# Kernel tuning notes

Measured on AMD Instinct MI355X. Metric: run time of the kernel, lower is better.

## Reference

```python
import jax, jax.numpy as jnp
import numpy as np

B, V = 4, 10242
N = B * V            # 40968 packed vertices
E_PER = 30720        # edges per mesh
HID = 128


def _bilinear_sample(fm, grid):
    """pytorch3d vert_align core: grid_sample(align_corners=True, bilinear).
    fm: [B,C,H,W], grid: [B,V,2] xy in [-1,1] -> [B,V,C]."""
    b_, c_, h_, w_ = fm.shape
    x = (grid[..., 0] + 1.0) * 0.5 * (w_ - 1)
    y = (grid[..., 1] + 1.0) * 0.5 * (h_ - 1)
    x0f, y0f = jnp.floor(x), jnp.floor(y)
    wx1, wy1 = x - x0f, y - y0f
    wx0, wy0 = 1.0 - wx1, 1.0 - wy1
    x0 = jnp.clip(x0f, 0, w_ - 1).astype(jnp.int32)
    x1 = jnp.clip(x0f + 1, 0, w_ - 1).astype(jnp.int32)
    y0 = jnp.clip(y0f, 0, h_ - 1).astype(jnp.int32)
    y1 = jnp.clip(y0f + 1, 0, h_ - 1).astype(jnp.int32)
    fmt = jnp.transpose(fm, (0, 2, 3, 1))  # [B,H,W,C]
    bi = jnp.arange(b_)[:, None]
    g = lambda yy, xx: fmt[bi, yy, xx]     # [B,V,C]
    return ((wy0 * wx0)[..., None] * g(y0, x0)
            + (wy0 * wx1)[..., None] * g(y0, x1)
            + (wy1 * wx0)[..., None] * g(y1, x0)
            + (wy1 * wx1)[..., None] * g(y1, x1))


def _graph_conv(x, edges, w0, b0, w1, b1):
    """pytorch3d GraphConv (undirected): W0 x_i + sum over both edge dirs of W1 x_j."""
    h0 = x @ w0 + b0
    h1 = x @ w1 + b1
    e0, e1 = edges[:, 0], edges[:, 1]
    agg = jnp.zeros_like(h0).at[e0].add(h1[e1]).at[e1].add(h1[e0])
    return h0 + agg


def setup_inputs() -> dict:
    key = jax.random.key(0)
    ks = jax.random.split(key, 20)
    s = 0.05
    # per-mesh edges, offset into packed index space
    e = jax.random.randint(ks[0], (B, E_PER, 2), 0, V)
    e = e + (jnp.arange(B) * V)[:, None, None]
    return {
        "feat1": jax.random.normal(ks[1], (B, 256, 56, 56), jnp.float32),
        "feat2": jax.random.normal(ks[2], (B, 512, 28, 28), jnp.float32),
        "feat3": jax.random.normal(ks[3], (B, 1024, 14, 14), jnp.float32),
        "feat4": jax.random.normal(ks[4], (B, 2048, 7, 7), jnp.float32),
        "aligned_verts": jax.random.uniform(ks[5], (B, V, 3), jnp.float32, -1.0, 1.0),
        "verts_packed": jax.random.normal(ks[6], (N, 3), jnp.float32),
        "image_enc": jax.random.normal(ks[7], (B, 256), jnp.float32),
        "edges": e.reshape(B * E_PER, 2).astype(jnp.int64),
        "bottleneck_w": jax.random.normal(ks[8], (3840, HID), jnp.float32) * s,
        "bottleneck_b": jnp.zeros((HID,), jnp.float32),
        "g0_w0": jax.random.normal(ks[9], (387, HID), jnp.float32) * s,
        "g0_b0": jnp.zeros((HID,), jnp.float32),
        "g0_w1": jax.random.normal(ks[10], (387, HID), jnp.float32) * s,
        "g0_b1": jnp.zeros((HID,), jnp.float32),
        "gw0": jax.random.normal(ks[11], (7, HID, HID), jnp.float32) * s,
        "gb0": jnp.zeros((7, HID), jnp.float32),
        "gw1": jax.random.normal(ks[12], (7, HID, HID), jnp.float32) * s,
        "gb1": jnp.zeros((7, HID), jnp.float32),
        "off_w": jax.random.normal(ks[13], (HID, 3), jnp.float32) * s,
        "off_b": jnp.zeros((3,), jnp.float32),
    }


def reference(feat1, feat2, feat3, feat4, aligned_verts, verts_packed, image_enc,
              edges, bottleneck_w, bottleneck_b, g0_w0, g0_b0, g0_w1, g0_b1,
              gw0, gb0, gw1, gb1, off_w, off_b):
    grid = aligned_verts[..., :2]  # vert_align uses xy only
    samp = jnp.concatenate([_bilinear_sample(f, grid)
                            for f in (feat1, feat2, feat3, feat4)], axis=-1)
    samp = samp.reshape(N, 3840)  # return_packed=True
    vfeat = jax.nn.relu(samp @ bottleneck_w + bottleneck_b)
    enc = jnp.repeat(image_enc, V, axis=0)  # repeat_interleave
    x = jnp.concatenate([vfeat, verts_packed, enc], axis=1)  # [N,387]
    x = jax.nn.relu(_graph_conv(x, edges, g0_w0, g0_b0, g0_w1, g0_b1))
    for i in range(7):
        x = jax.nn.relu(_graph_conv(x, edges, gw0[i], gb0[i], gw1[i], gb1[i]))
    return x @ off_w + off_b  # delta_v [N,3]
```

## Files before the change

### kernel.cpp

```cpp
#include <hip/hip_runtime.h>

static inline int ceil_div(int a, int b) { return (a + b - 1) / b; }

typedef __attribute__((ext_vector_type(8))) short short8;
typedef __attribute__((ext_vector_type(4))) float floatx4;

__device__ __forceinline__ unsigned short f2bf(float f) {
    unsigned int u = __float_as_uint(f);
    unsigned int r = (u + 0x7fffu + ((u >> 16) & 1u)) >> 16;
    return (unsigned short)r;
}
__device__ __forceinline__ float bf2f(unsigned short h) {
    return __uint_as_float(((unsigned int)h) << 16);
}

__global__ __launch_bounds__(1024) void scan1_k(const int* __restrict__ deg,
                                                int* __restrict__ excl,
                                                int* __restrict__ bsum, int Nv) {
    __shared__ int s[1024];
    int tid = threadIdx.x;
    int i = blockIdx.x * 1024 + tid;
    int v = (i < Nv) ? deg[i] : 0;
    s[tid] = v;
    __syncthreads();
    for (int off = 1; off < 1024; off <<= 1) {
        int t = (tid >= off) ? s[tid - off] : 0;
        __syncthreads();
        if (tid >= off) s[tid] += t;
        __syncthreads();
    }
    if (i < Nv) excl[i] = s[tid] - v;
    if (tid == 1023) bsum[blockIdx.x] = s[1023];
}

__global__ __launch_bounds__(64) void scan2_k(int* __restrict__ bsum, int nb) {
    __shared__ int s[64];
    int tid = threadIdx.x;
    int v = (tid < nb) ? bsum[tid] : 0;
    s[tid] = v;
    __syncthreads();
    for (int off = 1; off < 64; off <<= 1) {
        int t = (tid >= off) ? s[tid - off] : 0;
        __syncthreads();
        if (tid >= off) s[tid] += t;
        __syncthreads();
    }
    if (tid < nb) bsum[tid] = s[tid] - v;
}

__global__ __launch_bounds__(1024) void scan3_k(const int* __restrict__ excl,
                                                const int* __restrict__ bsum,
                                                const int* __restrict__ deg,
                                                int* __restrict__ rowptr,
                                                int* __restrict__ cursor, int Nv) {
    int i = blockIdx.x * 1024 + threadIdx.x;
    if (i < Nv) {
        int val = excl[i] + bsum[blockIdx.x];
        rowptr[i] = val;
        cursor[i] = val;
        if (i == Nv - 1) rowptr[Nv] = val + deg[i];
    }
}

__global__ __launch_bounds__(256) void fill_adj_k(const int* __restrict__ edges,
                                                  int* __restrict__ cursor,
                                                  int* __restrict__ adj, int E) {
    int e = blockIdx.x * blockDim.x + threadIdx.x;
    if (e < E) {
        int a = edges[2 * e], b = edges[2 * e + 1];
        adj[atomicAdd(&cursor[a], 1)] = b;
        adj[atomicAdd(&cursor[b], 1)] = a;
    }
}

__global__ __launch_bounds__(256) void fatpre_k(const int* __restrict__ edges,
                                                int* __restrict__ deg, int E, int nE,
                                                const float* __restrict__ g0w0,
                                                const float* __restrict__ g0w1,
                                                const float* __restrict__ gw0,
                                                const float* __restrict__ gw1,
                                                unsigned short* __restrict__ Wt,
                                                const float* __restrict__ bw,
                                                unsigned short* __restrict__ bwT,
                                                const float* __restrict__ enc,
                                                float* __restrict__ encp, int B_) {
    int bid = blockIdx.x;
    int tid = threadIdx.x;
    if (bid < nE) {
        int e = bid * 256 + tid;
        if (e < E) {
            atomicAdd(&deg[edges[2 * e]], 1);
            atomicAdd(&deg[edges[2 * e + 1]], 1);
        }
    } else if (bid < nE + 16) {
        int lh = bid - nE;
        int l = lh >> 1, h = lh & 1;
        const float* src;
        if (l == 0) src = h ? g0w1 : g0w0;
        else src = (h ? gw1 : gw0) + (size_t)(l - 1) * 16384;
        unsigned short* dst = Wt + (size_t)lh * 16384;
        for (int idx = tid; idx < 16384; idx += 256) {
            int n = idx >> 7, k = idx & 127;
            dst[n * 128 + k] = f2bf(src[k * 128 + n]);
        }
    } else if (bid < nE + 46) {
        int blk = bid - nE - 16;
        for (int idx = tid; idx < 16384; idx += 256) {
            int n = idx >> 7, kk = idx & 127;
            bwT[(size_t)n * 3840 + blk * 128 + kk] =
                f2bf(bw[(size_t)(blk * 128 + kk) * 128 + n]);
        }
    } else {
        int b = bid - nE - 46;
        int sH = tid >> 7;
        int j = tid & 127;
        const float* w = sH ? g0w1 : g0w0;
        const float* eb = enc + b * 256;
        float acc = 0.f;
        for (int c = 0; c < 256; ++c) acc = fmaf(eb[c], w[(131 + c) * 128 + j], acc);
        encp[(sH * B_ + b) * 128 + j] = acc;
    }
}

__global__ __launch_bounds__(256) void proj_all_k(
    const float* __restrict__ fm1, const float* __restrict__ fm2,
    const float* __restrict__ fm3, const float* __restrict__ fm4,
    const unsigned short* __restrict__ bwT, float* __restrict__ q1, float* __restrict__ q2,
    float* __restrict__ q3, float* __restrict__ q4, int B_) {
    __shared__ unsigned short wlds[8192];

    int tid = threadIdx.x;
    int n1 = 49 * B_ * 4, n2 = 13 * B_ * 8, n3 = 4 * B_ * 16;
    int bid = blockIdx.x;
    const float* fm;
    float* op;
    int C, HW, PT, idx, koff;
    if (bid < n1) {
        fm = fm1; op = q1; C = 256; HW = 3136; PT = 49; idx = bid; koff = 0;
    } else if (bid < n1 + n2) {
        fm = fm2; op = q2; C = 512; HW = 784; PT = 13; idx = bid - n1; koff = 256;
    } else if (bid < n1 + n2 + n3) {
        fm = fm3; op = q3; C = 1024; HW = 196; PT = 4; idx = bid - n1 - n2; koff = 768;
    } else {
        fm = fm4; op = q4; C = 2048; HW = 49; PT = 1; idx = bid - n1 - n2 - n3; koff = 1792;
    }
    int pt = idx % PT;
    int r2 = idx / PT;
    int b = r2 % B_;
    int zz = r2 / B_;
    int p0 = pt * 64;
    int S = B_ * HW * 128;
    const float* fmb = fm + (size_t)b * C * HW;
    int kcf = zz * 64;
    int kcw = koff + kcf;

#pragma unroll
    for (int l = 0; l < 4; ++l) {
        int i2 = tid + l * 256;
        int n = i2 >> 3, c16 = i2 & 7;
        *(short8*)&wlds[n * 64 + ((c16 ^ (n & 7)) * 8)] =
            *(const short8*)(bwT + (size_t)n * 3840 + kcw + c16 * 8);
    }

    int wave = tid >> 6, lane = tid & 63;
    int row16 = lane & 15, quad = lane >> 4;
    int p = p0 + wave * 16 + row16;
    bool pok = (p < HW);
    int pc = pok ? p : 0;
    short8 ax[2];
#pragma unroll
    for (int ks = 0; ks < 2; ++ks) {
#pragma unroll
        for (int j = 0; j < 8; ++j) {
            float v = pok ? fmb[(size_t)(kcf + ks * 32 + quad * 8 + j) * HW + pc] : 0.f;
            ax[ks][j] = (short)f2bf(v);
        }
    }
    __syncthreads();

    floatx4 acc[8];
#pragma unroll
    for (int j = 0; j < 8; ++j) acc[j] = (floatx4){0.f, 0.f, 0.f, 0.f};
#pragma unroll
    for (int ks = 0; ks < 2; ++ks) {
        int c = ks * 4 + quad;
#pragma unroll
        for (int nt = 0; nt < 8; ++nt) {
            int wr = nt * 16 + row16;
            short8 bwf = *(short8*)&wlds[wr * 64 + ((c ^ (wr & 7)) * 8)];
            acc[nt] = __builtin_amdgcn_mfma_f32_16x16x32_bf16(ax[ks], bwf, acc[nt], 0, 0, 0);
        }
    }

    float* obase = op + (size_t)zz * S + (size_t)b * HW * 128;
#pragma unroll
    for (int nt = 0; nt < 8; ++nt) {
        int colg = nt * 16 + row16;
#pragma unroll
        for (int rr = 0; rr < 4; ++rr) {
            int pr = p0 + wave * 16 + quad * 4 + rr;
            if (pr < HW) obase[(size_t)pr * 128 + colg] = acc[nt][rr];
        }
    }
}

__global__ __launch_bounds__(256) void reduce4_k(const float* __restrict__ q1,
                                                 const float* __restrict__ q2,
                                                 const float* __restrict__ q3,
                                                 const float* __restrict__ q4,
                                                 float* __restrict__ o1, float* __restrict__ o2,
                                                 float* __restrict__ o3, float* __restrict__ o4,
                                                 int S1, int S2, int S3, int S4) {
    int i = (blockIdx.x * 256 + threadIdx.x) * 4;
    const float* src;
    float* dst;
    int S, z, base;
    if (i < S1) {
        src = q1; dst = o1; S = S1; z = 4; base = i;
    } else if (i < S1 + S2) {
        src = q2; dst = o2; S = S2; z = 8; base = i - S1;
    } else if (i < S1 + S2 + S3) {
        src = q3; dst = o3; S = S3; z = 16; base = i - S1 - S2;
    } else if (i < S1 + S2 + S3 + S4) {
        src = q4; dst = o4; S = S4; z = 32; base = i - S1 - S2 - S3;
    } else {
        return;
    }
    float4 a = *(const float4*)(src + base);
    for (int zz = 1; zz < z; ++zz) {
        float4 b = *(const float4*)(src + (size_t)zz * S + base);
        a.x += b.x; a.y += b.y; a.z += b.z; a.w += b.w;
    }
    *(float4*)(dst + base) = a;
}

__device__ __forceinline__ float sample_level(const float* __restrict__ pp, int Hh, int Ww,
                                              float gx, float gy, int j) {
    float x = (gx + 1.f) * 0.5f * (float)(Ww - 1);
    float y = (gy + 1.f) * 0.5f * (float)(Hh - 1);
    float x0f = floorf(x), y0f = floorf(y);
    float wx1 = x - x0f, wy1 = y - y0f;
    float wx0 = 1.f - wx1, wy0 = 1.f - wy1;
    int x0 = (int)fminf(fmaxf(x0f, 0.f), (float)(Ww - 1));
    int x1 = (int)fminf(fmaxf(x0f + 1.f, 0.f), (float)(Ww - 1));
    int y0 = (int)fminf(fmaxf(y0f, 0.f), (float)(Hh - 1));
    int y1 = (int)fminf(fmaxf(y0f + 1.f, 0.f), (float)(Hh - 1));
    const float* r00 = pp + (size_t)(y0 * Ww + x0) * 128;
    const float* r01 = pp + (size_t)(y0 * Ww + x1) * 128;
    const float* r10 = pp + (size_t)(y1 * Ww + x0) * 128;
    const float* r11 = pp + (size_t)(y1 * Ww + x1) * 128;
    return wy0 * (wx0 * r00[j] + wx1 * r01[j]) + wy1 * (wx0 * r10[j] + wx1 * r11[j]);
}

__global__ __launch_bounds__(128) void sample_bottleneck_k(
    const float* __restrict__ av, const float* __restrict__ pp1, const float* __restrict__ pp2,
    const float* __restrict__ pp3, const float* __restrict__ pp4, const float* __restrict__ bb,
    const float* __restrict__ verts, const float* __restrict__ encp,
    const float* __restrict__ g0w0, const float* __restrict__ g0w1,
    const float* __restrict__ g0b0, const float* __restrict__ g0b1,
    unsigned short* __restrict__ X, unsigned short* __restrict__ H, int V_, int B_) {
    int n = blockIdx.x, j = threadIdx.x;
    int b = n / V_;
    float gx = av[(size_t)n * 3 + 0];
    float gy = av[(size_t)n * 3 + 1];
    float acc = bb[j];
    acc += sample_level(pp1 + (size_t)b * 3136 * 128, 56, 56, gx, gy, j);
    acc += sample_level(pp2 + (size_t)b * 784 * 128, 28, 28, gx, gy, j);
    acc += sample_level(pp3 + (size_t)b * 196 * 128, 14, 14, gx, gy, j);
    acc += sample_level(pp4 + (size_t)b * 49 * 128, 7, 7, gx, gy, j);
    X[(size_t)n * 128 + j] = f2bf(fmaxf(acc, 0.f));
    float v0 = verts[n * 3 + 0], v1 = verts[n * 3 + 1], v2 = verts[n * 3 + 2];
    float h0 = encp[(0 * B_ + b) * 128 + j] + g0b0[j] + v0 * g0w0[128 * 128 + j] +
               v1 * g0w0[129 * 128 + j] + v2 * g0w0[130 * 128 + j];
    float h1 = encp[(1 * B_ + b) * 128 + j] + g0b1[j] + v0 * g0w1[128 * 128 + j] +
               v1 * g0w1[129 * 128 + j] + v2 * g0w1[130 * 128 + j];
    H[(size_t)n * 256 + j] = f2bf(h0);
    H[(size_t)n * 256 + 128 + j] = f2bf(h1);
}

__device__ __forceinline__ int xcd_vertex(int bid, int wave, int V_, int B_, int Nv) {
    if (B_ == 4) {
        int xcd = bid & 7;
        int lb = (bid >> 3) * 2 + (xcd & 1);
        int lv = lb * 4 + wave;
        if (lv >= V_) return -1;
        return (xcd >> 1) * V_ + lv;
    }
    int n = bid * 4 + wave;
    return (n < Nv) ? n : -1;
}

__global__ __launch_bounds__(256) void aggpre_k(const unsigned short* __restrict__ H,
                                                const int* __restrict__ rowptr,
                                                const int* __restrict__ adj,
                                                float* __restrict__ pre, int Nv, int V_,
                                                int B_) {
    int wave = threadIdx.x >> 6, lane = threadIdx.x & 63;
    int n = xcd_vertex(blockIdx.x, wave, V_, B_, Nv);
    if (n < 0) return;
    unsigned int u = *(const unsigned int*)(H + (size_t)n * 256 + 2 * lane);
    float a0 = bf2f((unsigned short)(u & 0xffff));
    float a1 = bf2f((unsigned short)(u >> 16));
    int s = rowptr[n], e = rowptr[n + 1];
    for (int t = s; t < e; t += 8) {
        int nb[8];
        unsigned int w[8];
#pragma unroll
        for (int q = 0; q < 8; ++q) {
            int idx = (t + q < e) ? (t + q) : (e - 1);
            nb[q] = adj[idx];
        }
#pragma unroll
        for (int q = 0; q < 8; ++q)
            w[q] = *(const unsigned int*)(H + (size_t)nb[q] * 256 + 128 + 2 * lane);
#pragma unroll
        for (int q = 0; q < 8; ++q) {
            if (t + q < e) {
                a0 += bf2f((unsigned short)(w[q] & 0xffff));
                a1 += bf2f((unsigned short)(w[q] >> 16));
            }
        }
    }
    pre[(size_t)n * 128 + 2 * lane] = a0;
    pre[(size_t)n * 128 + 2 * lane + 1] = a1;
}

__global__ __launch_bounds__(256) void agg_x_k(const unsigned short* __restrict__ X,
                                               const int* __restrict__ rowptr,
                                               const int* __restrict__ adj,
                                               unsigned short* __restrict__ Agg, int Nv,
                                               int V_, int B_) {
    int wave = threadIdx.x >> 6, lane = threadIdx.x & 63;
    int n = xcd_vertex(blockIdx.x, wave, V_, B_, Nv);
    if (n < 0) return;
    const unsigned int* Xu = (const unsigned int*)X;
    float a0 = 0.f, a1 = 0.f;
    int s = rowptr[n], e = rowptr[n + 1];
    for (int t = s; t < e; t += 8) {
        int nb[8];
        unsigned int w[8];
#pragma unroll
        for (int q = 0; q < 8; ++q) {
            int idx = (t + q < e) ? (t + q) : (e - 1);
            nb[q] = adj[idx];
        }
#pragma unroll
        for (int q = 0; q < 8; ++q) w[q] = Xu[(size_t)nb[q] * 64 + lane];
#pragma unroll
        for (int q = 0; q < 8; ++q) {
            if (t + q < e) {
                a0 += bf2f((unsigned short)(w[q] & 0xffff));
                a1 += bf2f((unsigned short)(w[q] >> 16));
            }
        }
    }
    unsigned int o = (unsigned int)f2bf(a0) | ((unsigned int)f2bf(a1) << 16);
    *(unsigned int*)(Agg + (size_t)n * 128 + 2 * lane) = o;
}

__global__ __launch_bounds__(256, 3) void gemm_dual_k(
    const unsigned short* __restrict__ Xin, const unsigned short* __restrict__ Agg,
    const unsigned short* __restrict__ Wt,
    const float* __restrict__ b0, const float* __restrict__ b1,
    const float* __restrict__ pre, const int* __restrict__ degv,
    unsigned short* __restrict__ Xout, int M) {
    __shared__ unsigned short wlds[16384];
    __shared__ unsigned short cs[64 * 72];
    __shared__ float bS[128];

    int tid = threadIdx.x;
    int m0 = blockIdx.x * 128;
    int yb = blockIdx.y;

    int wave = tid >> 6, lane = tid & 63;
    int row16 = lane & 15;
    int quad = lane >> 4;
    int wrow = wave * 16;

    short8 axT[2][4], agT[2][4];
    int dgT[2][4];
    {
        int g = min(m0 + wrow + row16, M - 1);
#pragma unroll
        for (int ks = 0; ks < 4; ++ks) {
            int koff = ks * 32 + quad * 8;
            axT[0][ks] = *(const short8*)(Xin + (size_t)g * 128 + koff);
            agT[0][ks] = *(const short8*)(Agg + (size_t)g * 128 + koff);
        }
#pragma unroll
        for (int rr = 0; rr < 4; ++rr)
            dgT[0][rr] = degv[min(m0 + wrow + quad * 4 + rr, M - 1)];
    }

    if (tid < 64) {
        bS[tid] = b0 ? b0[yb * 64 + tid] : 0.f;
        bS[64 + tid] = b1 ? b1[yb * 64 + tid] : 0.f;
    }

    const unsigned short* W0h = Wt + (size_t)yb * 64 * 128;
    const unsigned short* W1h = Wt + 16384 + (size_t)yb * 64 * 128;
#pragma unroll
    for (int l = 0; l < 8; ++l) {
        int idx = tid + l * 256;
        int half = idx >> 10;
        int r = (idx >> 4) & 63;
        int c16 = idx & 15;
        int sw = (c16 ^ (r & 15)) * 8;
        const unsigned short* src = (half ? W1h : W0h) + r * 128 + c16 * 8;
        *(short8*)&wlds[half * 8192 + r * 128 + sw] = *(const short8*)src;
    }
    __syncthreads();

    {
        int g = min(m0 + 64 + wrow + row16, M - 1);
#pragma unroll
        for (int ks = 0; ks < 4; ++ks) {
            int koff = ks * 32 + quad * 8;
            axT[1][ks] = *(const short8*)(Xin + (size_t)g * 128 + koff);
            agT[1][ks] = *(const short8*)(Agg + (size_t)g * 128 + koff);
        }
#pragma unroll
        for (int rr = 0; rr < 4; ++rr)
            dgT[1][rr] = degv[min(m0 + 64 + wrow + quad * 4 + rr, M - 1)];
    }

#pragma unroll
    for (int t = 0; t < 2; ++t) {
        int mT = m0 + t * 64;
        floatx4 acc[4];
#pragma unroll
        for (int j = 0; j < 4; j++) acc[j] = (floatx4){0.f, 0.f, 0.f, 0.f};

#pragma unroll
        for (int ks = 0; ks < 4; ++ks) {
            int c = ks * 4 + quad;
#pragma unroll
            for (int nt = 0; nt < 4; ++nt) {
                int wr = nt * 16 + row16;
                short8 bw0 = *(short8*)&wlds[wr * 128 + ((c ^ row16) * 8)];
                short8 bw1 = *(short8*)&wlds[8192 + wr * 128 + ((c ^ row16) * 8)];
                acc[nt] = __builtin_amdgcn_mfma_f32_16x16x32_bf16(axT[t][ks], bw0, acc[nt], 0, 0, 0);
                acc[nt] = __builtin_amdgcn_mfma_f32_16x16x32_bf16(agT[t][ks], bw1, acc[nt], 0, 0, 0);
            }
        }

#pragma unroll
        for (int nt = 0; nt < 4; ++nt) {
            int colh = nt * 16 + row16;
            int colg = yb * 64 + colh;
            float bc0 = bS[colh];
            float bc1 = bS[64 + colh];
#pragma unroll
            for (int rr = 0; rr < 4; ++rr) {
                int row = wrow + quad * 4 + rr;
                int gm = mT + row;
                float v = acc[nt][rr] + bc0 + (float)dgT[t][rr] * bc1;
                if (pre && gm < M) v += pre[(size_t)gm * 128 + colg];
                cs[row * 72 + colh] = f2bf(fmaxf(v, 0.f));
            }
        }
        __syncthreads();

        {
            int r = tid >> 2;
            int cq = (tid & 3) * 16;
            int gm = mT + r;
            if (gm < M) {
                unsigned short* dst = Xout + (size_t)gm * 128 + yb * 64 + cq;
                *(short8*)dst = *(short8*)&cs[r * 72 + cq];
                *(short8*)(dst + 8) = *(short8*)&cs[r * 72 + cq + 8];
            }
        }
        __syncthreads();
    }
}

__global__ __launch_bounds__(256) void head_k(const unsigned short* __restrict__ X,
                                              const float* __restrict__ off_w,
                                              const float* __restrict__ off_b,
                                              float* __restrict__ out, int Nv) {
    int wave = threadIdx.x >> 6, lane = threadIdx.x & 63;
    int n = blockIdx.x * 4 + wave;
    if (n >= Nv) return;
    unsigned int u = *(const unsigned int*)(X + (size_t)n * 128 + 2 * lane);
    float x0 = bf2f((unsigned short)(u & 0xffff));
    float x1 = bf2f((unsigned short)(u >> 16));
    int c0 = 2 * lane, c1 = 2 * lane + 1;
    float p0 = x0 * off_w[c0 * 3 + 0] + x1 * off_w[c1 * 3 + 0];
    float p1 = x0 * off_w[c0 * 3 + 1] + x1 * off_w[c1 * 3 + 1];
    float p2 = x0 * off_w[c0 * 3 + 2] + x1 * off_w[c1 * 3 + 2];
#pragma unroll
    for (int m = 1; m < 64; m <<= 1) {
        p0 += __shfl_xor(p0, m);
        p1 += __shfl_xor(p1, m);
        p2 += __shfl_xor(p2, m);
    }
    if (lane == 0) {
        out[n * 3 + 0] = p0 + off_b[0];
        out[n * 3 + 1] = p1 + off_b[1];
        out[n * 3 + 2] = p2 + off_b[2];
    }
}

extern "C" void kernel_launch(void* const* d_in, const int* in_sizes, int n_in, void* d_out,
                              int out_size, void* d_ws, size_t ws_size, hipStream_t stream) {
    const float* feat1 = (const float*)d_in[0];
    const float* feat2 = (const float*)d_in[1];
    const float* feat3 = (const float*)d_in[2];
    const float* feat4 = (const float*)d_in[3];
    const float* av = (const float*)d_in[4];
    const float* verts = (const float*)d_in[5];
    const float* image_enc = (const float*)d_in[6];
    const int* edges = (const int*)d_in[7];
    const float* bw = (const float*)d_in[8];
    const float* bb = (const float*)d_in[9];
    const float* g0w0 = (const float*)d_in[10];
    const float* g0b0 = (const float*)d_in[11];
    const float* g0w1 = (const float*)d_in[12];
    const float* g0b1 = (const float*)d_in[13];
    const float* gw0 = (const float*)d_in[14];
    const float* gb0 = (const float*)d_in[15];
    const float* gw1 = (const float*)d_in[16];
    const float* gb1 = (const float*)d_in[17];
    const float* off_w = (const float*)d_in[18];
    const float* off_b = (const float*)d_in[19];

    int B_ = in_sizes[6] / 256;
    int N_ = in_sizes[5] / 3;
    int V_ = N_ / B_;
    int E_ = in_sizes[7] / 2;

    char* wsb = (char*)d_ws;
    size_t off = 0;
    auto alloc = [&](size_t bytes) -> void* {
        void* p = (void*)(wsb + off);
        off += (bytes + 255) & ~(size_t)255;
        return p;
    };
    int S1 = B_ * 3136 * 128;
    int S2 = B_ * 784 * 128;
    int S3 = B_ * 196 * 128;
    int S4 = B_ * 49 * 128;
    float* pp1 = (float*)alloc((size_t)S1 * 4);
    float* pp2 = (float*)alloc((size_t)S2 * 4);
    float* pp3 = (float*)alloc((size_t)S3 * 4);
    float* pp4 = (float*)alloc((size_t)S4 * 4);
    float* q1 = (float*)alloc((size_t)4 * S1 * 4);
    float* q2 = (float*)alloc((size_t)8 * S2 * 4);
    float* q3 = (float*)alloc((size_t)16 * S3 * 4);
    float* q4 = (float*)alloc((size_t)32 * S4 * 4);
    unsigned short* XA = (unsigned short*)alloc((size_t)N_ * 128 * 2);
    unsigned short* XB = (unsigned short*)alloc((size_t)N_ * 128 * 2);
    unsigned short* AggB = (unsigned short*)alloc((size_t)N_ * 128 * 2);
    unsigned short* Hb = (unsigned short*)alloc((size_t)N_ * 256 * 2);
    float* pre = (float*)alloc((size_t)N_ * 128 * 4);
    unsigned short* Wt = (unsigned short*)alloc((size_t)8 * 2 * 128 * 128 * 2);
    unsigned short* bwT = (unsigned short*)alloc((size_t)128 * 3840 * 2);
    float* encp = (float*)alloc((size_t)2 * B_ * 128 * 4);
    int* deg = (int*)alloc((size_t)(N_ + 1) * 4);
    int* rowptr = (int*)alloc((size_t)(N_ + 1) * 4);
    int* cursor = (int*)alloc((size_t)N_ * 4);
    int* excl = (int*)alloc((size_t)N_ * 4);
    int* bsum = (int*)alloc((size_t)64 * 4);
    int* adj = (int*)alloc((size_t)2 * E_ * 4);

    hipMemsetAsync(deg, 0, (N_ + 1) * sizeof(int), stream);

    int nE = ceil_div(E_, 256);
    fatpre_k<<<nE + 46 + B_, 256, 0, stream>>>(edges, deg, E_, nE, g0w0, g0w1, gw0, gw1, Wt,
                                               bw, bwT, image_enc, encp, B_);

    int nb = ceil_div(N_, 1024);
    scan1_k<<<nb, 1024, 0, stream>>>(deg, excl, bsum, N_);
    scan2_k<<<1, 64, 0, stream>>>(bsum, nb);
    scan3_k<<<nb, 1024, 0, stream>>>(excl, bsum, deg, rowptr, cursor, N_);
    fill_adj_k<<<ceil_div(E_, 256), 256, 0, stream>>>(edges, cursor, adj, E_);

    int nproj = 49 * B_ * 4 + 13 * B_ * 8 + 4 * B_ * 16 + 1 * B_ * 32;
    proj_all_k<<<nproj, 256, 0, stream>>>(feat1, feat2, feat3, feat4, bwT, q1, q2, q3, q4, B_);
    int tot4 = (S1 + S2 + S3 + S4) / 4;
    reduce4_k<<<ceil_div(tot4, 256), 256, 0, stream>>>(q1, q2, q3, q4, pp1, pp2, pp3, pp4, S1,
                                                       S2, S3, S4);

    sample_bottleneck_k<<<N_, 128, 0, stream>>>(av, pp1, pp2, pp3, pp4, bb, verts, encp, g0w0,
                                                g0w1, g0b0, g0b1, XA, Hb, V_, B_);

    int agrid = (B_ == 4) ? 8 * ceil_div(ceil_div(V_, 4), 2) : ceil_div(N_, 4);

    aggpre_k<<<agrid, 256, 0, stream>>>(Hb, rowptr, adj, pre, N_, V_, B_);

    dim3 ggrid(ceil_div(N_, 128), 2);
    agg_x_k<<<agrid, 256, 0, stream>>>(XA, rowptr, adj, AggB, N_, V_, B_);
    gemm_dual_k<<<ggrid, 256, 0, stream>>>(XA, AggB, Wt, nullptr, nullptr, pre, deg, XB, N_);
    unsigned short* Xc = XB;
    unsigned short* Xn = XA;
    for (int i = 0; i < 7; ++i) {
        agg_x_k<<<agrid, 256, 0, stream>>>(Xc, rowptr, adj, AggB, N_, V_, B_);
        gemm_dual_k<<<ggrid, 256, 0, stream>>>(Xc, AggB, Wt + (size_t)(i + 1) * 32768,
                                               gb0 + i * 128, gb1 + i * 128, nullptr, deg, Xn,
                                               N_);
        unsigned short* t = Xc;
        Xc = Xn;
        Xn = t;
    }
    head_k<<<ceil_div(N_, 4), 256, 0, stream>>>(Xc, off_w, off_b, (float*)d_out, N_);
}
```

Baseline: 476.4 us.

## Fuse neighbor aggregation into layer GEMM and drop split-K projection reduce

Each graph-conv layer now gathers neighbor features straight into shared memory inside the GEMM kernel, with a wave-level CSR walk, instead of writing an Agg buffer from a separate kernel. This removes a launch and a global round trip per layer. The feature-map projection loops over all K chunks inside one block instead of writing split-K partials and reducing them in a second kernel. The cost is fewer, longer projection blocks with less parallelism, and aggregation work that is duplicated across the two column-half blocks of each layer.

```diff
diff --git a/kernel.cpp b/kernel.cpp
--- a/kernel.cpp
+++ b/kernel.cpp
@@ -125,74 +125,75 @@
 __global__ __launch_bounds__(256) void proj_all_k(
     const float* __restrict__ fm1, const float* __restrict__ fm2,
     const float* __restrict__ fm3, const float* __restrict__ fm4,
-    const unsigned short* __restrict__ bwT, float* __restrict__ q1, float* __restrict__ q2,
-    float* __restrict__ q3, float* __restrict__ q4, int B_) {
+    const unsigned short* __restrict__ bwT, float* __restrict__ o1, float* __restrict__ o2,
+    float* __restrict__ o3, float* __restrict__ o4, int B_) {
     __shared__ unsigned short wlds[8192];
 
     int tid = threadIdx.x;
-    int n1 = 49 * B_ * 4, n2 = 13 * B_ * 8, n3 = 4 * B_ * 16;
+    int n1 = 49 * B_, n2 = 13 * B_, n3 = 4 * B_;
     int bid = blockIdx.x;
     const float* fm;
     float* op;
     int C, HW, PT, idx, koff;
     if (bid < n1) {
-        fm = fm1; op = q1; C = 256; HW = 3136; PT = 49; idx = bid; koff = 0;
+        fm = fm1; op = o1; C = 256; HW = 3136; PT = 49; idx = bid; koff = 0;
     } else if (bid < n1 + n2) {
-        fm = fm2; op = q2; C = 512; HW = 784; PT = 13; idx = bid - n1; koff = 256;
+        fm = fm2; op = o2; C = 512; HW = 784; PT = 13; idx = bid - n1; koff = 256;
     } else if (bid < n1 + n2 + n3) {
-        fm = fm3; op = q3; C = 1024; HW = 196; PT = 4; idx = bid - n1 - n2; koff = 768;
+        fm = fm3; op = o3; C = 1024; HW = 196; PT = 4; idx = bid - n1 - n2; koff = 768;
     } else {
-        fm = fm4; op = q4; C = 2048; HW = 49; PT = 1; idx = bid - n1 - n2 - n3; koff = 1792;
+        fm = fm4; op = o4; C = 2048; HW = 49; PT = 1; idx = bid - n1 - n2 - n3; koff = 1792;
     }
     int pt = idx % PT;
-    int r2 = idx / PT;
-    int b = r2 % B_;
-    int zz = r2 / B_;
+    int b = idx / PT;
     int p0 = pt * 64;
-    int S = B_ * HW * 128;
     const float* fmb = fm + (size_t)b * C * HW;
-    int kcf = zz * 64;
-    int kcw = koff + kcf;
-
-#pragma unroll
-    for (int l = 0; l < 4; ++l) {
-        int i2 = tid + l * 256;
-        int n = i2 >> 3, c16 = i2 & 7;
-        *(short8*)&wlds[n * 64 + ((c16 ^ (n & 7)) * 8)] =
-            *(const short8*)(bwT + (size_t)n * 3840 + kcw + c16 * 8);
-    }
 
     int wave = tid >> 6, lane = tid & 63;
     int row16 = lane & 15, quad = lane >> 4;
     int p = p0 + wave * 16 + row16;
     bool pok = (p < HW);
     int pc = pok ? p : 0;
-    short8 ax[2];
-#pragma unroll
-    for (int ks = 0; ks < 2; ++ks) {
-#pragma unroll
-        for (int j = 0; j < 8; ++j) {
-            float v = pok ? fmb[(size_t)(kcf + ks * 32 + quad * 8 + j) * HW + pc] : 0.f;
-            ax[ks][j] = (short)f2bf(v);
-        }
-    }
-    __syncthreads();
 
     floatx4 acc[8];
 #pragma unroll
     for (int j = 0; j < 8; ++j) acc[j] = (floatx4){0.f, 0.f, 0.f, 0.f};
-#pragma unroll
-    for (int ks = 0; ks < 2; ++ks) {
-        int c = ks * 4 + quad;
-#pragma unroll
-        for (int nt = 0; nt < 8; ++nt) {
-            int wr = nt * 16 + row16;
-            short8 bwf = *(short8*)&wlds[wr * 64 + ((c ^ (wr & 7)) * 8)];
-            acc[nt] = __builtin_amdgcn_mfma_f32_16x16x32_bf16(ax[ks], bwf, acc[nt], 0, 0, 0);
-        }
-    }
-
-    float* obase = op + (size_t)zz * S + (size_t)b * HW * 128;
+
+    int nz = C >> 6;
+    for (int z = 0; z < nz; ++z) {
+        int kcf = z * 64;
+        int kcw = koff + kcf;
+        __syncthreads();
+#pragma unroll
+        for (int l = 0; l < 4; ++l) {
+            int i2 = tid + l * 256;
+            int n = i2 >> 3, c16 = i2 & 7;
+            *(short8*)&wlds[n * 64 + ((c16 ^ (n & 7)) * 8)] =
+                *(const short8*)(bwT + (size_t)n * 3840 + kcw + c16 * 8);
+        }
+        short8 ax[2];
+#pragma unroll
+        for (int ks = 0; ks < 2; ++ks) {
+#pragma unroll
+            for (int j = 0; j < 8; ++j) {
+                float v = pok ? fmb[(size_t)(kcf + ks * 32 + quad * 8 + j) * HW + pc] : 0.f;
+                ax[ks][j] = (short)f2bf(v);
+            }
+        }
+        __syncthreads();
+#pragma unroll
+        for (int ks = 0; ks < 2; ++ks) {
+            int c = ks * 4 + quad;
+#pragma unroll
+            for (int nt = 0; nt < 8; ++nt) {
+                int wr = nt * 16 + row16;
+                short8 bwf = *(short8*)&wlds[wr * 64 + ((c ^ (wr & 7)) * 8)];
+                acc[nt] = __builtin_amdgcn_mfma_f32_16x16x32_bf16(ax[ks], bwf, acc[nt], 0, 0, 0);
+            }
+        }
+    }
+
+    float* obase = op + (size_t)b * HW * 128;
 #pragma unroll
     for (int nt = 0; nt < 8; ++nt) {
         int colg = nt * 16 + row16;
@@ -202,36 +203,6 @@
             if (pr < HW) obase[(size_t)pr * 128 + colg] = acc[nt][rr];
         }
     }
-}
-
-__global__ __launch_bounds__(256) void reduce4_k(const float* __restrict__ q1,
-                                                 const float* __restrict__ q2,
-                                                 const float* __restrict__ q3,
-                                                 const float* __restrict__ q4,
-                                                 float* __restrict__ o1, float* __restrict__ o2,
-                                                 float* __restrict__ o3, float* __restrict__ o4,
-                                                 int S1, int S2, int S3, int S4) {
-    int i = (blockIdx.x * 256 + threadIdx.x) * 4;
-    const float* src;
-    float* dst;
-    int S, z, base;
-    if (i < S1) {
-        src = q1; dst = o1; S = S1; z = 4; base = i;
-    } else if (i < S1 + S2) {
-        src = q2; dst = o2; S = S2; z = 8; base = i - S1;
-    } else if (i < S1 + S2 + S3) {
-        src = q3; dst = o3; S = S3; z = 16; base = i - S1 - S2;
-    } else if (i < S1 + S2 + S3 + S4) {
-        src = q4; dst = o4; S = S4; z = 32; base = i - S1 - S2 - S3;
-    } else {
-        return;
-    }
-    float4 a = *(const float4*)(src + base);
-    for (int zz = 1; zz < z; ++zz) {
-        float4 b = *(const float4*)(src + (size_t)zz * S + base);
-        a.x += b.x; a.y += b.y; a.z += b.z; a.w += b.w;
-    }
-    *(float4*)(dst + base) = a;
 }
 
 __device__ __forceinline__ float sample_level(const float* __restrict__ pp, int Hh, int Ww,
@@ -325,71 +296,53 @@
     pre[(size_t)n * 128 + 2 * lane + 1] = a1;
 }
 
-__global__ __launch_bounds__(256) void agg_x_k(const unsigned short* __restrict__ X,
-                                               const int* __restrict__ rowptr,
-                                               const int* __restrict__ adj,
-                                               unsigned short* __restrict__ Agg, int Nv,
-                                               int V_, int B_) {
-    int wave = threadIdx.x >> 6, lane = threadIdx.x & 63;
-    int n = xcd_vertex(blockIdx.x, wave, V_, B_, Nv);
-    if (n < 0) return;
-    const unsigned int* Xu = (const unsigned int*)X;
-    float a0 = 0.f, a1 = 0.f;
-    int s = rowptr[n], e = rowptr[n + 1];
-    for (int t = s; t < e; t += 8) {
-        int nb[8];
-        unsigned int w[8];
-#pragma unroll
-        for (int q = 0; q < 8; ++q) {
-            int idx = (t + q < e) ? (t + q) : (e - 1);
-            nb[q] = adj[idx];
-        }
-#pragma unroll
-        for (int q = 0; q < 8; ++q) w[q] = Xu[(size_t)nb[q] * 64 + lane];
-#pragma unroll
-        for (int q = 0; q < 8; ++q) {
-            if (t + q < e) {
-                a0 += bf2f((unsigned short)(w[q] & 0xffff));
-                a1 += bf2f((unsigned short)(w[q] >> 16));
-            }
-        }
-    }
-    unsigned int o = (unsigned int)f2bf(a0) | ((unsigned int)f2bf(a1) << 16);
-    *(unsigned int*)(Agg + (size_t)n * 128 + 2 * lane) = o;
-}
-
-__global__ __launch_bounds__(256, 3) void gemm_dual_k(
-    const unsigned short* __restrict__ Xin, const unsigned short* __restrict__ Agg,
+__global__ __launch_bounds__(256, 2) void layer_k(
+    const unsigned short* __restrict__ Xin, const int* __restrict__ rowptr,
+    const int* __restrict__ adj,
     const unsigned short* __restrict__ Wt,
     const float* __restrict__ b0, const float* __restrict__ b1,
     const float* __restrict__ pre, const int* __restrict__ degv,
-    unsigned short* __restrict__ Xout, int M) {
+    unsigned short* __restrict__ Xout, int V_, int B_, int TB) {
     __shared__ unsigned short wlds[16384];
-    __shared__ unsigned short cs[64 * 72];
+    __shared__ unsigned short aggs[16384];
     __shared__ float bS[128];
 
+    int x = blockIdx.x, yb = blockIdx.y;
+    int b, lt;
+    if (B_ == 4) {
+        int xcd = x & 7;
+        b = xcd >> 1;
+        lt = (x >> 3) * 2 + (xcd & 1);
+    } else {
+        b = x / TB;
+        lt = x % TB;
+    }
+    if (lt >= TB) return;
+    int m0 = b * V_ + lt * 128;
+    int bEnd = (b + 1) * V_;
+    int vrows = min(128, V_ - lt * 128);
+
     int tid = threadIdx.x;
-    int m0 = blockIdx.x * 128;
-    int yb = blockIdx.y;
-
     int wave = tid >> 6, lane = tid & 63;
     int row16 = lane & 15;
     int quad = lane >> 4;
-    int wrow = wave * 16;
-
-    short8 axT[2][4], agT[2][4];
+
+    int gbase = m0 + wave * 32;
+    int rend_l = rowptr[min(gbase + 1 + lane, bEnd)];
+    int sWv = rowptr[min(gbase, bEnd)];
+    int eWv = __shfl(rend_l, 31);
+
+    short8 axT[2][4];
     int dgT[2][4];
-    {
-        int g = min(m0 + wrow + row16, M - 1);
-#pragma unroll
-        for (int ks = 0; ks < 4; ++ks) {
-            int koff = ks * 32 + quad * 8;
-            axT[0][ks] = *(const short8*)(Xin + (size_t)g * 128 + koff);
-            agT[0][ks] = *(const short8*)(Agg + (size_t)g * 128 + koff);
-        }
+#pragma unroll
+    for (int t = 0; t < 2; ++t) {
+        int g = min(m0 + t * 64 + wave * 16 + row16, bEnd - 1);
+#pragma unroll
+        for (int ks = 0; ks < 4; ++ks)
+            axT[t][ks] = *(const short8*)(Xin + (size_t)g * 128 + ks * 32 + quad * 8);
 #pragma unroll
         for (int rr = 0; rr < 4; ++rr)
-            dgT[0][rr] = degv[min(m0 + wrow + quad * 4 + rr, M - 1)];
+            dgT[t][rr] = degv[min(m0 + t * 64 + wave * 16 + quad * 4 + rr, bEnd - 1)];
     }
 
     if (tid < 64) {
@@ -409,41 +362,87 @@
         const unsigned short* src = (half ? W1h : W0h) + r * 128 + c16 * 8;
         *(short8*)&wlds[half * 8192 + r * 128 + sw] = *(const short8*)src;
     }
+
+    {
+        const unsigned int* Xu = (const unsigned int*)Xin;
+        float a0 = 0.f, a1 = 0.f;
+        int r = 0;
+        int nextEnd = __shfl(rend_l, 0);
+        auto flush = [&](int rloc, float v0, float v1) {
+            unsigned int o = (unsigned int)f2bf(v0) | ((unsigned int)f2bf(v1) << 16);
+            int rl = wave * 32 + rloc;
+            *(unsigned int*)&aggs[rl * 128 + (((lane >> 2) ^ (rl & 15)) * 8) +
+                                  (lane & 3) * 2] = o;
+        };
+        for (int t = sWv; t < eWv; t += 8) {
+            int nb[8];
+            unsigned int w[8];
+#pragma unroll
+            for (int q = 0; q < 8; ++q) {
+                int idx = (t + q < eWv) ? (t + q) : (eWv - 1);
+                nb[q] = adj[idx];
+            }
+#pragma unroll
+            for (int q = 0; q < 8; ++q) w[q] = Xu[(size_t)nb[q] * 64 + lane];
+#pragma unroll
+            for (int q = 0; q < 8; ++q) {
+                int pos = t + q;
+                if (pos < eWv) {
+                    while (pos >= nextEnd) {
+                        flush(r, a0, a1);
+                        a0 = 0.f;
+                        a1 = 0.f;
+                        ++r;
+                        nextEnd = __shfl(rend_l, r);
+                    }
+                    a0 += bf2f((unsigned short)(w[q] & 0xffff));
+                    a1 += bf2f((unsigned short)(w[q] >> 16));
+                }
+            }
+        }
+        while (r < 32) {
+            flush(r, a0, a1);
+            a0 = 0.f;
+            a1 = 0.f;
+            ++r;
+        }
+    }
     __syncthreads();
 
-    {
-        int g = min(m0 + 64 + wrow + row16, M - 1);
-#pragma unroll
-        for (int ks = 0; ks < 4; ++ks) {
-            int koff = ks * 32 + quad * 8;
-            axT[1][ks] = *(const short8*)(Xin + (size_t)g * 128 + koff);
-            agT[1][ks] = *(const short8*)(Agg + (size_t)g * 128 + koff);
-        }
-#pragma unroll
-        for (int rr = 0; rr < 4; ++rr)
-            dgT[1][rr] = degv[min(m0 + 64 + wrow + quad * 4 + rr, M - 1)];
-    }
-
+    floatx4 acc[2][4];
+#pragma unroll
+    for (int t = 0; t < 2; ++t)
+#pragma unroll
+        for (int j = 0; j < 4; ++j) acc[t][j] = (floatx4){0.f, 0.f, 0.f, 0.f};
+
+#pragma unroll
+    for (int ks = 0; ks < 4; ++ks) {
+        int c = ks * 4 + quad;
+        short8 agf[2];
+#pragma unroll
+        for (int t = 0; t < 2; ++t) {
+            int rlA = t * 64 + wave * 16 + row16;
+            agf[t] = *(short8*)&aggs[rlA * 128 + ((c ^ row16) * 8)];
+        }
+#pragma unroll
+        for (int nt = 0; nt < 4; ++nt) {
+            int wr = nt * 16 + row16;
+            short8 bw0 = *(short8*)&wlds[wr * 128 + ((c ^ row16) * 8)];
+            short8 bw1 = *(short8*)&wlds[8192 + wr * 128 + ((c ^ row16) * 8)];
+#pragma unroll
+            for (int t = 0; t < 2; ++t) {
+                acc[t][nt] =
+                    __builtin_amdgcn_mfma_f32_16x16x32_bf16(axT[t][ks], bw0, acc[t][nt], 0, 0, 0);
+                acc[t][nt] =
+                    __builtin_amdgcn_mfma_f32_16x16x32_bf16(agf[t], bw1, acc[t][nt], 0, 0, 0);
+            }
+        }
+    }
+    __syncthreads();
+
+    unsigned short* cs = aggs;
 #pragma unroll
     for (int t = 0; t < 2; ++t) {
-        int mT = m0 + t * 64;
-        floatx4 acc[4];
-#pragma unroll
-        for (int j = 0; j < 4; j++) acc[j] = (floatx4){0.f, 0.f, 0.f, 0.f};
-
-#pragma unroll
-        for (int ks = 0; ks < 4; ++ks) {
-            int c = ks * 4 + quad;
-#pragma unroll
-            for (int nt = 0; nt < 4; ++nt) {
-                int wr = nt * 16 + row16;
-                short8 bw0 = *(short8*)&wlds[wr * 128 + ((c ^ row16) * 8)];
-                short8 bw1 = *(short8*)&wlds[8192 + wr * 128 + ((c ^ row16) * 8)];
-                acc[nt] = __builtin_amdgcn_mfma_f32_16x16x32_bf16(axT[t][ks], bw0, acc[nt], 0, 0, 0);
-                acc[nt] = __builtin_amdgcn_mfma_f32_16x16x32_bf16(agT[t][ks], bw1, acc[nt], 0, 0, 0);
-            }
-        }
-
 #pragma unroll
         for (int nt = 0; nt < 4; ++nt) {
             int colh = nt * 16 + row16;
@@ -452,26 +451,24 @@
             float bc1 = bS[64 + colh];
 #pragma unroll
             for (int rr = 0; rr < 4; ++rr) {
-                int row = wrow + quad * 4 + rr;
-                int gm = mT + row;
-                float v = acc[nt][rr] + bc0 + (float)dgT[t][rr] * bc1;
-                if (pre && gm < M) v += pre[(size_t)gm * 128 + colg];
+                int row = t * 64 + wave * 16 + quad * 4 + rr;
+                float v = acc[t][nt][rr] + bc0 + (float)dgT[t][rr] * bc1;
+                if (pre && row < vrows) v += pre[(size_t)(m0 + row) * 128 + colg];
                 cs[row * 72 + colh] = f2bf(fmaxf(v, 0.f));
             }
         }
-        __syncthreads();
-
-        {
-            int r = tid >> 2;
-            int cq = (tid & 3) * 16;
-            int gm = mT + r;
-            if (gm < M) {
-                unsigned short* dst = Xout + (size_t)gm * 128 + yb * 64 + cq;
-                *(short8*)dst = *(short8*)&cs[r * 72 + cq];
-                *(short8*)(dst + 8) = *(short8*)&cs[r * 72 + cq + 8];
-            }
-        }
-        __syncthreads();
+    }
+    __syncthreads();
+
+    {
+        int r = tid >> 1;
+        if (r < vrows) {
+            int ch = (tid & 1) * 32;
+            unsigned short* dst = Xout + (size_t)(m0 + r) * 128 + yb * 64 + ch;
+#pragma unroll
+            for (int cc = 0; cc < 4; ++cc)
+                *(short8*)(dst + cc * 8) = *(short8*)&cs[r * 72 + ch + cc * 8];
+        }
     }
 }
 
@@ -545,13 +542,8 @@
     float* pp2 = (float*)alloc((size_t)S2 * 4);
     float* pp3 = (float*)alloc((size_t)S3 * 4);
     float* pp4 = (float*)alloc((size_t)S4 * 4);
-    float* q1 = (float*)alloc((size_t)4 * S1 * 4);
-    float* q2 = (float*)alloc((size_t)8 * S2 * 4);
-    float* q3 = (float*)alloc((size_t)16 * S3 * 4);
-    float* q4 = (float*)alloc((size_t)32 * S4 * 4);
     unsigned short* XA = (unsigned short*)alloc((size_t)N_ * 128 * 2);
     unsigned short* XB = (unsigned short*)alloc((size_t)N_ * 128 * 2);
-    unsigned short* AggB = (unsigned short*)alloc((size_t)N_ * 128 * 2);
     unsigned short* Hb = (unsigned short*)alloc((size_t)N_ * 256 * 2);
     float* pre = (float*)alloc((size_t)N_ * 128 * 4);
     unsigned short* Wt = (unsigned short*)alloc((size_t)8 * 2 * 128 * 128 * 2);
@@ -576,29 +568,26 @@
     scan3_k<<<nb, 1024, 0, stream>>>(excl, bsum, deg, rowptr, cursor, N_);
     fill_adj_k<<<ceil_div(E_, 256), 256, 0, stream>>>(edges, cursor, adj, E_);
 
-    int nproj = 49 * B_ * 4 + 13 * B_ * 8 + 4 * B_ * 16 + 1 * B_ * 32;
-    proj_all_k<<<nproj, 256, 0, stream>>>(feat1, feat2, feat3, feat4, bwT, q1, q2, q3, q4, B_);
-    int tot4 = (S1 + S2 + S3 + S4) / 4;
-    reduce4_k<<<ceil_div(tot4, 256), 256, 0, stream>>>(q1, q2, q3, q4, pp1, pp2, pp3, pp4, S1,
-                                                       S2, S3, S4);
+    int nproj = (49 + 13 + 4 + 1) * B_;
+    proj_all_k<<<nproj, 256, 0, stream>>>(feat1, feat2, feat3, feat4, bwT, pp1, pp2, pp3, pp4,
+                                          B_);
 
     sample_bottleneck_k<<<N_, 128, 0, stream>>>(av, pp1, pp2, pp3, pp4, bb, verts, encp, g0w0,
                                                 g0w1, g0b0, g0b1, XA, Hb, V_, B_);
 
     int agrid = (B_ == 4) ? 8 * ceil_div(ceil_div(V_, 4), 2) : ceil_div(N_, 4);
-
     aggpre_k<<<agrid, 256, 0, stream>>>(Hb, rowptr, adj, pre, N_, V_, B_);
 
-    dim3 ggrid(ceil_div(N_, 128), 2);
-    agg_x_k<<<agrid, 256, 0, stream>>>(XA, rowptr, adj, AggB, N_, V_, B_);
-    gemm_dual_k<<<ggrid, 256, 0, stream>>>(XA, AggB, Wt, nullptr, nullptr, pre, deg, XB, N_);
+    int TB = ceil_div(V_, 128);
+    dim3 lgrid((B_ == 4) ? 8 * ceil_div(TB, 2) : B_ * TB, 2);
+    layer_k<<<lgrid, 256, 0, stream>>>(XA, rowptr, adj, Wt, nullptr, nullptr, pre, deg, XB, V_,
+                                       B_, TB);
     unsigned short* Xc = XB;
     unsigned short* Xn = XA;
     for (int i = 0; i < 7; ++i) {
-        agg_x_k<<<agrid, 256, 0, stream>>>(Xc, rowptr, adj, AggB, N_, V_, B_);
-        gemm_dual_k<<<ggrid, 256, 0, stream>>>(Xc, AggB, Wt + (size_t)(i + 1) * 32768,
-                                               gb0 + i * 128, gb1 + i * 128, nullptr, deg, Xn,
-                                               N_);
+        layer_k<<<lgrid, 256, 0, stream>>>(Xc, rowptr, adj, Wt + (size_t)(i + 1) * 32768,
+                                           gb0 + i * 128, gb1 + i * 128, nullptr, deg, Xn, V_,
+                                           B_, TB);
         unsigned short* t = Xc;
         Xc = Xn;
         Xn = t;
```

Result: slower. 740.2 us (+55.4%).
